# Optimization experiments

Hardware: AMD Instinct MI355X
Metric: run time of the kernel (lower is better)

## Reference

```python
import jax, jax.numpy as jnp
import numpy as np

B, L, N = 512, 512, 128


def setup_inputs() -> dict:
    key = jax.random.key(0)
    k1, k2, k3, k4 = jax.random.split(key, 4)
    emission = jax.random.normal(k1, (B, L, N), dtype=jnp.float32)
    target = jax.random.randint(k2, (B, L), 0, N, dtype=jnp.int32)
    mask = jnp.ones((B, L), dtype=jnp.float32)
    # params: uniform(-0.1, 0.1) as in reset_parameters
    start_trans = jax.random.uniform(k3, (N,), minval=-0.1, maxval=0.1, dtype=jnp.float32)
    trans = jax.random.uniform(k4, (N, N), minval=-0.1, maxval=0.1, dtype=jnp.float32)
    return {"emission": emission, "target": target, "mask": mask,
            "start_trans": start_trans, "trans": trans}


def _normalizer(emission, mask, start_trans, trans):
    # scores: [B, N]
    scores0 = start_trans + emission[:, 0]
    em_t = jnp.swapaxes(emission, 0, 1)[1:]          # [L-1, B, N]
    m_t = jnp.swapaxes(mask, 0, 1)[1:, :, None]      # [L-1, B, 1]

    def step(scores, xs):
        em_i, m_i = xs
        nxt = jax.nn.logsumexp(scores[:, :, None] + trans[None], axis=1) + em_i
        nxt = m_i * nxt + (1.0 - m_i) * scores
        return nxt, None

    final, _ = jax.lax.scan(step, scores0, (em_t, m_t))
    return jax.nn.logsumexp(final, axis=1)            # [B]


def _path_score(emission, target, mask, start_trans, trans):
    # mask*next + (1-mask)*scores == scores + mask*increment -> fully vectorizable
    b = jnp.arange(emission.shape[0])
    t0 = target[:, 0]
    s0 = start_trans[t0] + emission[b, 0, t0]                         # [B]
    prev, cur = target[:, :-1], target[:, 1:]                         # [B, L-1]
    em_gather = jnp.take_along_axis(emission[:, 1:], cur[:, :, None], axis=2)[..., 0]
    inc = trans[prev, cur] + em_gather                                # [B, L-1]
    return s0 + jnp.sum(mask[:, 1:] * inc, axis=1)                    # [B]


def reference(emission, target, mask, start_trans, trans):
    path_scores = _path_score(emission, target, mask, start_trans, trans)
    normalizer = _normalizer(emission, mask, start_trans, trans)
    return jnp.mean(normalizer - path_scores)
```

## Files before the change

### kernel.cpp

```cpp
#include <hip/hip_runtime.h>

#define B_ 512
#define L_ 512
#define N_ 128
#define TM 256
#define C_BIAS 3.0f

typedef _Float16 h2_t __attribute__((ext_vector_type(2)));
typedef _Float16 h8_t __attribute__((ext_vector_type(8)));
typedef float    f4_t __attribute__((ext_vector_type(4)));

#define DPP_STEP_MAX(v, ctrl)                                                   \
    {                                                                           \
        int _t = __builtin_amdgcn_update_dpp(__float_as_int(v),                 \
                    __float_as_int(v), ctrl, 0xf, 0xf, false);                  \
        v = fmaxf(v, __int_as_float(_t));                                       \
    }
#define DPP_STEP_ADD(v, ctrl)                                                   \
    {                                                                           \
        int _t = __builtin_amdgcn_update_dpp(__float_as_int(v),                 \
                    __float_as_int(v), ctrl, 0xf, 0xf, false);                  \
        v = v + __int_as_float(_t);                                             \
    }

__device__ __forceinline__ float wave_max(float v) {
    DPP_STEP_MAX(v, 0xB1);
    DPP_STEP_MAX(v, 0x4E);
    DPP_STEP_MAX(v, 0x141);
    DPP_STEP_MAX(v, 0x140);
    DPP_STEP_MAX(v, 0x142);
    DPP_STEP_MAX(v, 0x143);
    return __int_as_float(__builtin_amdgcn_readlane(__float_as_int(v), 63));
}
__device__ __forceinline__ float wave_sum(float v) {
    DPP_STEP_ADD(v, 0xB1);
    DPP_STEP_ADD(v, 0x4E);
    DPP_STEP_ADD(v, 0x141);
    DPP_STEP_ADD(v, 0x140);
    DPP_STEP_ADD(v, 0x142);
    DPP_STEP_ADD(v, 0x143);
    return __int_as_float(__builtin_amdgcn_readlane(__float_as_int(v), 63));
}

__global__ __launch_bounds__(64) void norm_kernel(
    const float* __restrict__ em, const int* __restrict__ tg,
    const float* __restrict__ mask, const float* __restrict__ st,
    const float* __restrict__ trans,
    float* __restrict__ alpha, float* __restrict__ beta,
    float* __restrict__ pathf, float* __restrict__ pathb)
{
    __shared__ __align__(16) _Float16 Eh[128];
    __shared__ __align__(8)  float    Sl[128];
    __shared__ float Mlds[TM];

    const int l  = threadIdx.x;
    const int c  = l & 15;
    const int h  = l >> 4;
    const int b  = blockIdx.x >> 1;
    const int bw = blockIdx.x & 1;
    const size_t base = (size_t)b * L_ * N_;
    const int bL = b * L_;

    if (bw == 0) {
        float pacc = 0.f;
        for (int t = 1 + l; t < TM; t += 64) {
            int cur  = tg[bL + t];
            int prev = tg[bL + t - 1];
            pacc += mask[bL + t] * (trans[prev * N_ + cur] + em[base + (size_t)t * N_ + cur]);
        }
        pacc = wave_sum(pacc);
        if (l == 0) {
            int t0 = tg[bL];
            pathf[b] = pacc + st[t0] + em[base + t0];
        }

#pragma unroll
        for (int k = 0; k < 4; ++k) Mlds[l + 64 * k] = mask[bL + l + 64 * k];

        h8_t Bf[8][4];
#pragma unroll
        for (int jt = 0; jt < 8; ++jt)
#pragma unroll
            for (int ks = 0; ks < 4; ++ks) {
                h8_t f;
#pragma unroll
                for (int e = 0; e < 8; ++e)
                    f[e] = (_Float16)__expf(trans[(32 * ks + 8 * h + e) * N_ + 16 * jt + c]);
                Bf[jt][ks] = f;
            }

        float2 e0 = *(const float2*)(em + base + 2 * l);
        float2 s2 = *(const float2*)(st + 2 * l);
        float ns0 = s2.x + e0.x;
        float ns1 = s2.y + e0.y;
        float Mprev = wave_max(fmaxf(ns0, ns1));
        {
            h2_t eo;
            eo[0] = (_Float16)__expf(ns0 - Mprev - C_BIAS);
            eo[1] = (_Float16)__expf(ns1 - Mprev - C_BIAS);
            ((h2_t*)Eh)[l] = eo;
        }

        float2 pipe0 = *(const float2*)(em + base + (size_t)1 * N_ + 2 * l);
        float2 pipe1 = *(const float2*)(em + base + (size_t)2 * N_ + 2 * l);
        float2 pipe2 = *(const float2*)(em + base + (size_t)3 * N_ + 2 * l);
        float2 pipe3 = *(const float2*)(em + base + (size_t)4 * N_ + 2 * l);

        auto step = [&](int t, float2& slot) {
            float2 emv = slot;
            int tpf = t + 4; if (tpf > TM - 1) tpf = TM - 1;
            slot = *(const float2*)(em + base + (size_t)tpf * N_ + 2 * l);
            float mk = Mlds[t];

            float mx = wave_max(fmaxf(ns0, ns1));

            const _Float16* Eb = (const _Float16*)Eh;
            h8_t A0 = *(const h8_t*)(Eb + 8 * h);
            h8_t A1 = *(const h8_t*)(Eb + 32 + 8 * h);
            h8_t A2 = *(const h8_t*)(Eb + 64 + 8 * h);
            h8_t A3 = *(const h8_t*)(Eb + 96 + 8 * h);

            f4_t z = {0.f, 0.f, 0.f, 0.f};
            f4_t acc[8];
#pragma unroll
            for (int jt = 0; jt < 8; ++jt) {
                f4_t a = __builtin_amdgcn_mfma_f32_16x16x32_f16(A0, Bf[jt][0], z, 0, 0, 0);
                a = __builtin_amdgcn_mfma_f32_16x16x32_f16(A1, Bf[jt][1], a, 0, 0, 0);
                a = __builtin_amdgcn_mfma_f32_16x16x32_f16(A2, Bf[jt][2], a, 0, 0, 0);
                a = __builtin_amdgcn_mfma_f32_16x16x32_f16(A3, Bf[jt][3], a, 0, 0, 0);
                acc[jt] = a;
            }
            if (l < 16) {
#pragma unroll
                for (int jt = 0; jt < 8; ++jt) Sl[16 * jt + c] = acc[jt][0];
            }
            float2 sv = *(const float2*)(Sl + 2 * l);

            float badd = Mprev + C_BIAS;
            float nxt0 = __logf(sv.x) + badd + emv.x;
            float nxt1 = __logf(sv.y) + badd + emv.y;
            float im = 1.f - mk;
            ns0 = mk * nxt0 + im * ns0;
            ns1 = mk * nxt1 + im * ns1;

            Mprev = mx;
            h2_t eo;
            eo[0] = (_Float16)__expf(ns0 - mx - C_BIAS);
            eo[1] = (_Float16)__expf(ns1 - mx - C_BIAS);
            ((h2_t*)Eh)[l] = eo;
        };

        for (int tt = 1; tt + 3 < TM; tt += 4) {
            step(tt    , pipe0);
            step(tt + 1, pipe1);
            step(tt + 2, pipe2);
            step(tt + 3, pipe3);
        }
        step(TM - 3, pipe0);
        step(TM - 2, pipe1);
        step(TM - 1, pipe2);

        *(float2*)(alpha + b * N_ + 2 * l) = make_float2(ns0, ns1);
    } else {
        float pacc = 0.f;
        for (int t = TM + l; t < L_; t += 64) {
            int cur  = tg[bL + t];
            int prev = tg[bL + t - 1];
            pacc += mask[bL + t] * (trans[prev * N_ + cur] + em[base + (size_t)t * N_ + cur]);
        }
        pacc = wave_sum(pacc);
        if (l == 0) pathb[b] = pacc;

#pragma unroll
        for (int k = 0; k < 4; ++k) Mlds[l + 64 * k] = mask[bL + TM + l + 64 * k];

        h8_t Bf[8][4];
#pragma unroll
        for (int it = 0; it < 8; ++it)
#pragma unroll
            for (int ks = 0; ks < 4; ++ks) {
                const float* p = trans + (size_t)(16 * it + c) * N_ + 32 * ks + 8 * h;
                float4 q0 = *(const float4*)p;
                float4 q1 = *(const float4*)(p + 4);
                h8_t f;
                f[0] = (_Float16)__expf(q0.x); f[1] = (_Float16)__expf(q0.y);
                f[2] = (_Float16)__expf(q0.z); f[3] = (_Float16)__expf(q0.w);
                f[4] = (_Float16)__expf(q1.x); f[5] = (_Float16)__expf(q1.y);
                f[6] = (_Float16)__expf(q1.z); f[7] = (_Float16)__expf(q1.w);
                Bf[it][ks] = f;
            }

        float2 e0 = *(const float2*)(em + base + (size_t)(L_ - 1) * N_ + 2 * l);
        float b0 = 0.f, b1 = 0.f;
        float v0 = e0.x, v1 = e0.y;
        float Mprev = wave_max(fmaxf(v0, v1));
        {
            h2_t eo;
            eo[0] = (_Float16)__expf(v0 - Mprev - C_BIAS);
            eo[1] = (_Float16)__expf(v1 - Mprev - C_BIAS);
            ((h2_t*)Eh)[l] = eo;
        }

        float2 pipe0 = *(const float2*)(em + base + (size_t)510 * N_ + 2 * l);
        float2 pipe1 = *(const float2*)(em + base + (size_t)509 * N_ + 2 * l);
        float2 pipe2 = *(const float2*)(em + base + (size_t)508 * N_ + 2 * l);
        float2 pipe3 = *(const float2*)(em + base + (size_t)507 * N_ + 2 * l);

        auto step = [&](int t, float2& slot) {
            float2 emt = slot;
            int tpf = t - 4; if (tpf < TM - 1) tpf = TM - 1;
            slot = *(const float2*)(em + base + (size_t)tpf * N_ + 2 * l);
            float mk = Mlds[t + 1 - TM];

            float mx = wave_max(fmaxf(v0, v1));

            const _Float16* Fb = (const _Float16*)Eh;
            h8_t A0 = *(const h8_t*)(Fb + 8 * h);
            h8_t A1 = *(const h8_t*)(Fb + 32 + 8 * h);
            h8_t A2 = *(const h8_t*)(Fb + 64 + 8 * h);
            h8_t A3 = *(const h8_t*)(Fb + 96 + 8 * h);

            f4_t z = {0.f, 0.f, 0.f, 0.f};
            f4_t acc[8];
#pragma unroll
            for (int it = 0; it < 8; ++it) {
                f4_t a = __builtin_amdgcn_mfma_f32_16x16x32_f16(A0, Bf[it][0], z, 0, 0, 0);
                a = __builtin_amdgcn_mfma_f32_16x16x32_f16(A1, Bf[it][1], a, 0, 0, 0);
                a = __builtin_amdgcn_mfma_f32_16x16x32_f16(A2, Bf[it][2], a, 0, 0, 0);
                a = __builtin_amdgcn_mfma_f32_16x16x32_f16(A3, Bf[it][3], a, 0, 0, 0);
                acc[it] = a;
            }
            if (l < 16) {
#pragma unroll
                for (int it = 0; it < 8; ++it) Sl[16 * it + c] = acc[it][0];
            }
            float2 sv = *(const float2*)(Sl + 2 * l);

            float badd = Mprev + C_BIAS;
            float upd0 = __logf(sv.x) + badd;
            float upd1 = __logf(sv.y) + badd;
            float im = 1.f - mk;
            b0 = mk * upd0 + im * b0;
            b1 = mk * upd1 + im * b1;

            v0 = b0 + emt.x;
            v1 = b1 + emt.y;
            Mprev = mx;
            h2_t eo;
            eo[0] = (_Float16)__expf(v0 - mx - C_BIAS);
            eo[1] = (_Float16)__expf(v1 - mx - C_BIAS);
            ((h2_t*)Eh)[l] = eo;
        };

        for (int tt = 510; tt >= 258; tt -= 4) {
            step(tt    , pipe0);
            step(tt - 1, pipe1);
            step(tt - 2, pipe2);
            step(tt - 3, pipe3);
        }

        *(float2*)(beta + b * N_ + 2 * l) = make_float2(b0, b1);
    }
}

__global__ __launch_bounds__(64) void zres_kernel(
    const float* __restrict__ alpha, const float* __restrict__ beta,
    const float* __restrict__ pathf, const float* __restrict__ pathb,
    float* __restrict__ zres)
{
    const int l = threadIdx.x;
    const int b = blockIdx.x;
    float2 av = *(const float2*)(alpha + b * N_ + 2 * l);
    float2 bv = *(const float2*)(beta  + b * N_ + 2 * l);
    float v0 = av.x + bv.x;
    float v1 = av.y + bv.y;
    float m = wave_max(fmaxf(v0, v1));
    float s = wave_sum(__expf(v0 - m) + __expf(v1 - m));
    if (l == 0) zres[b] = m + __logf(s) - pathf[b] - pathb[b];
}

__global__ __launch_bounds__(64) void mean_kernel(
    const float* __restrict__ zres, float* __restrict__ out)
{
    const int l = threadIdx.x;
    const float4* z4 = (const float4*)zres;
    float4 a = z4[2 * l];
    float4 c = z4[2 * l + 1];
    float acc = ((a.x + a.y) + (a.z + a.w)) + ((c.x + c.y) + (c.z + c.w));
    acc = wave_sum(acc);
    if (l == 0) out[0] = acc * (1.0f / (float)B_);
}

extern "C" void kernel_launch(void* const* d_in, const int* in_sizes, int n_in,
                              void* d_out, int out_size, void* d_ws, size_t ws_size,
                              hipStream_t stream) {
    const float* emission    = (const float*)d_in[0];
    const int*   target      = (const int*)  d_in[1];
    const float* mask        = (const float*)d_in[2];
    const float* start_trans = (const float*)d_in[3];
    const float* trans       = (const float*)d_in[4];
    float* out = (float*)d_out;

    float* ws_f  = (float*)d_ws;
    float* alpha = ws_f;
    float* beta  = ws_f + B_ * N_;
    float* pathf = ws_f + 2 * B_ * N_;
    float* pathb = ws_f + 2 * B_ * N_ + B_;
    float* zres  = ws_f + 2 * B_ * N_ + 2 * B_;

    norm_kernel<<<2 * B_, 64, 0, stream>>>(emission, target, mask, start_trans,
                                           trans, alpha, beta, pathf, pathb);
    zres_kernel<<<B_, 64, 0, stream>>>(alpha, beta, pathf, pathb, zres);
    mean_kernel<<<1, 64, 0, stream>>>(zres, out);
}
```

Before: 302.7 us.

## Remap state ownership to MFMA output layout, drop LDS round-trip for scores

Each lane now owns the two states (32*h+c and +16) that match the MFMA accumulator layout, so results are taken straight from the accumulator registers with selects. This removes the per-step LDS scatter of accumulator results and the gather that read them back, which sat on the serial recurrence path. Emission loads become scalar loads with a strided pattern instead of float2, and launch bounds add a min-blocks hint. In exchange, Eh writes become two half-word stores per lane.

New measurement: 307.7 us. About the same (+1.7%).

```diff
diff --git a/kernel.cpp b/kernel.cpp
--- a/kernel.cpp
+++ b/kernel.cpp
@@ -42,7 +42,13 @@
     return __int_as_float(__builtin_amdgcn_readlane(__float_as_int(v), 63));
 }
 
-__global__ __launch_bounds__(64) void norm_kernel(
+#define CHAIN4(qv, BT)                                                          \
+    f4_t qv = __builtin_amdgcn_mfma_f32_16x16x32_f16(A0, BT[0], z, 0, 0, 0);    \
+    qv = __builtin_amdgcn_mfma_f32_16x16x32_f16(A1, BT[1], qv, 0, 0, 0);        \
+    qv = __builtin_amdgcn_mfma_f32_16x16x32_f16(A2, BT[2], qv, 0, 0, 0);        \
+    qv = __builtin_amdgcn_mfma_f32_16x16x32_f16(A3, BT[3], qv, 0, 0, 0);
+
+__global__ __launch_bounds__(64, 1) void norm_kernel(
     const float* __restrict__ em, const int* __restrict__ tg,
     const float* __restrict__ mask, const float* __restrict__ st,
     const float* __restrict__ trans,
@@ -50,12 +56,15 @@
     float* __restrict__ pathf, float* __restrict__ pathb)
 {
     __shared__ __align__(16) _Float16 Eh[128];
-    __shared__ __align__(8)  float    Sl[128];
     __shared__ float Mlds[TM];
 
     const int l  = threadIdx.x;
     const int c  = l & 15;
     const int h  = l >> 4;
+    const int s0 = 32 * h + c;
+    const int s1 = s0 + 16;
+    const bool hb0 = (h & 1) != 0;
+    const bool hb1 = (h & 2) != 0;
     const int b  = blockIdx.x >> 1;
     const int bw = blockIdx.x & 1;
     const size_t base = (size_t)b * L_ * N_;
@@ -89,27 +98,22 @@
                 Bf[jt][ks] = f;
             }
 
-        float2 e0 = *(const float2*)(em + base + 2 * l);
-        float2 s2 = *(const float2*)(st + 2 * l);
-        float ns0 = s2.x + e0.x;
-        float ns1 = s2.y + e0.y;
+        float ns0 = st[s0] + em[base + s0];
+        float ns1 = st[s1] + em[base + s1];
         float Mprev = wave_max(fmaxf(ns0, ns1));
-        {
-            h2_t eo;
-            eo[0] = (_Float16)__expf(ns0 - Mprev - C_BIAS);
-            eo[1] = (_Float16)__expf(ns1 - Mprev - C_BIAS);
-            ((h2_t*)Eh)[l] = eo;
-        }
-
-        float2 pipe0 = *(const float2*)(em + base + (size_t)1 * N_ + 2 * l);
-        float2 pipe1 = *(const float2*)(em + base + (size_t)2 * N_ + 2 * l);
-        float2 pipe2 = *(const float2*)(em + base + (size_t)3 * N_ + 2 * l);
-        float2 pipe3 = *(const float2*)(em + base + (size_t)4 * N_ + 2 * l);
-
-        auto step = [&](int t, float2& slot) {
-            float2 emv = slot;
+        Eh[s0] = (_Float16)__expf(ns0 - Mprev - C_BIAS);
+        Eh[s1] = (_Float16)__expf(ns1 - Mprev - C_BIAS);
+
+        float pa0 = em[base + (size_t)1 * N_ + s0], pb0 = em[base + (size_t)1 * N_ + s1];
+        float pa1 = em[base + (size_t)2 * N_ + s0], pb1 = em[base + (size_t)2 * N_ + s1];
+        float pa2 = em[base + (size_t)3 * N_ + s0], pb2 = em[base + (size_t)3 * N_ + s1];
+        float pa3 = em[base + (size_t)4 * N_ + s0], pb3 = em[base + (size_t)4 * N_ + s1];
+
+        auto step = [&](int t, float& sa, float& sb) {
+            float emv0 = sa, emv1 = sb;
             int tpf = t + 4; if (tpf > TM - 1) tpf = TM - 1;
-            slot = *(const float2*)(em + base + (size_t)tpf * N_ + 2 * l);
+            sa = em[base + (size_t)tpf * N_ + s0];
+            sb = em[base + (size_t)tpf * N_ + s1];
             float mk = Mlds[t];
 
             float mx = wave_max(fmaxf(ns0, ns1));
@@ -121,46 +125,36 @@
             h8_t A3 = *(const h8_t*)(Eb + 96 + 8 * h);
 
             f4_t z = {0.f, 0.f, 0.f, 0.f};
-            f4_t acc[8];
-#pragma unroll
-            for (int jt = 0; jt < 8; ++jt) {
-                f4_t a = __builtin_amdgcn_mfma_f32_16x16x32_f16(A0, Bf[jt][0], z, 0, 0, 0);
-                a = __builtin_amdgcn_mfma_f32_16x16x32_f16(A1, Bf[jt][1], a, 0, 0, 0);
-                a = __builtin_amdgcn_mfma_f32_16x16x32_f16(A2, Bf[jt][2], a, 0, 0, 0);
-                a = __builtin_amdgcn_mfma_f32_16x16x32_f16(A3, Bf[jt][3], a, 0, 0, 0);
-                acc[jt] = a;
-            }
-            if (l < 16) {
-#pragma unroll
-                for (int jt = 0; jt < 8; ++jt) Sl[16 * jt + c] = acc[jt][0];
-            }
-            float2 sv = *(const float2*)(Sl + 2 * l);
+            CHAIN4(q0, Bf[0]) CHAIN4(q1, Bf[1]) CHAIN4(q2, Bf[2]) CHAIN4(q3, Bf[3])
+            CHAIN4(q4, Bf[4]) CHAIN4(q5, Bf[5]) CHAIN4(q6, Bf[6]) CHAIN4(q7, Bf[7])
+
+            float sv0 = hb1 ? (hb0 ? q6[0] : q4[0]) : (hb0 ? q2[0] : q0[0]);
+            float sv1 = hb1 ? (hb0 ? q7[0] : q5[0]) : (hb0 ? q3[0] : q1[0]);
 
             float badd = Mprev + C_BIAS;
-            float nxt0 = __logf(sv.x) + badd + emv.x;
-            float nxt1 = __logf(sv.y) + badd + emv.y;
+            float nxt0 = __logf(sv0) + badd + emv0;
+            float nxt1 = __logf(sv1) + badd + emv1;
             float im = 1.f - mk;
             ns0 = mk * nxt0 + im * ns0;
             ns1 = mk * nxt1 + im * ns1;
 
             Mprev = mx;
-            h2_t eo;
-            eo[0] = (_Float16)__expf(ns0 - mx - C_BIAS);
-            eo[1] = (_Float16)__expf(ns1 - mx - C_BIAS);
-            ((h2_t*)Eh)[l] = eo;
+            Eh[s0] = (_Float16)__expf(ns0 - mx - C_BIAS);
+            Eh[s1] = (_Float16)__expf(ns1 - mx - C_BIAS);
         };
 
         for (int tt = 1; tt + 3 < TM; tt += 4) {
-            step(tt    , pipe0);
-            step(tt + 1, pipe1);
-            step(tt + 2, pipe2);
-            step(tt + 3, pipe3);
-        }
-        step(TM - 3, pipe0);
-        step(TM - 2, pipe1);
-        step(TM - 1, pipe2);
-
-        *(float2*)(alpha + b * N_ + 2 * l) = make_float2(ns0, ns1);
+            step(tt    , pa0, pb0);
+            step(tt + 1, pa1, pb1);
+            step(tt + 2, pa2, pb2);
+            step(tt + 3, pa3, pb3);
+        }
+        step(TM - 3, pa0, pb0);
+        step(TM - 2, pa1, pb1);
+        step(TM - 1, pa2, pb2);
+
+        alpha[b * N_ + s0] = ns0;
+        alpha[b * N_ + s1] = ns1;
     } else {
         float pacc = 0.f;
         for (int t = TM + l; t < L_; t += 64) {
@@ -190,26 +184,23 @@
                 Bf[it][ks] = f;
             }
 
-        float2 e0 = *(const float2*)(em + base + (size_t)(L_ - 1) * N_ + 2 * l);
         float b0 = 0.f, b1 = 0.f;
-        float v0 = e0.x, v1 = e0.y;
+        float v0 = em[base + (size_t)(L_ - 1) * N_ + s0];
+        float v1 = em[base + (size_t)(L_ - 1) * N_ + s1];
         float Mprev = wave_max(fmaxf(v0, v1));
-        {
-            h2_t eo;
-            eo[0] = (_Float16)__expf(v0 - Mprev - C_BIAS);
-            eo[1] = (_Float16)__expf(v1 - Mprev - C_BIAS);
-            ((h2_t*)Eh)[l] = eo;
-        }
-
-        float2 pipe0 = *(const float2*)(em + base + (size_t)510 * N_ + 2 * l);
-        float2 pipe1 = *(const float2*)(em + base + (size_t)509 * N_ + 2 * l);
-        float2 pipe2 = *(const float2*)(em + base + (size_t)508 * N_ + 2 * l);
-        float2 pipe3 = *(const float2*)(em + base + (size_t)507 * N_ + 2 * l);
-
-        auto step = [&](int t, float2& slot) {
-            float2 emt = slot;
+        Eh[s0] = (_Float16)__expf(v0 - Mprev - C_BIAS);
+        Eh[s1] = (_Float16)__expf(v1 - Mprev - C_BIAS);
+
+        float pa0 = em[base + (size_t)510 * N_ + s0], pb0 = em[base + (size_t)510 * N_ + s1];
+        float pa1 = em[base + (size_t)509 * N_ + s0], pb1 = em[base + (size_t)509 * N_ + s1];
+        float pa2 = em[base + (size_t)508 * N_ + s0], pb2 = em[base + (size_t)508 * N_ + s1];
+        float pa3 = em[base + (size_t)507 * N_ + s0], pb3 = em[base + (size_t)507 * N_ + s1];
+
+        auto step = [&](int t, float& sa, float& sb) {
+            float emt0 = sa, emt1 = sb;
             int tpf = t - 4; if (tpf < TM - 1) tpf = TM - 1;
-            slot = *(const float2*)(em + base + (size_t)tpf * N_ + 2 * l);
+            sa = em[base + (size_t)tpf * N_ + s0];
+            sb = em[base + (size_t)tpf * N_ + s1];
             float mk = Mlds[t + 1 - TM];
 
             float mx = wave_max(fmaxf(v0, v1));
@@ -221,45 +212,35 @@
             h8_t A3 = *(const h8_t*)(Fb + 96 + 8 * h);
 
             f4_t z = {0.f, 0.f, 0.f, 0.f};
-            f4_t acc[8];
-#pragma unroll
-            for (int it = 0; it < 8; ++it) {
-                f4_t a = __builtin_amdgcn_mfma_f32_16x16x32_f16(A0, Bf[it][0], z, 0, 0, 0);
-                a = __builtin_amdgcn_mfma_f32_16x16x32_f16(A1, Bf[it][1], a, 0, 0, 0);
-                a = __builtin_amdgcn_mfma_f32_16x16x32_f16(A2, Bf[it][2], a, 0, 0, 0);
-                a = __builtin_amdgcn_mfma_f32_16x16x32_f16(A3, Bf[it][3], a, 0, 0, 0);
-                acc[it] = a;
-            }
-            if (l < 16) {
-#pragma unroll
-                for (int it = 0; it < 8; ++it) Sl[16 * it + c] = acc[it][0];
-            }
-            float2 sv = *(const float2*)(Sl + 2 * l);
+            CHAIN4(q0, Bf[0]) CHAIN4(q1, Bf[1]) CHAIN4(q2, Bf[2]) CHAIN4(q3, Bf[3])
+            CHAIN4(q4, Bf[4]) CHAIN4(q5, Bf[5]) CHAIN4(q6, Bf[6]) CHAIN4(q7, Bf[7])
+
+            float sv0 = hb1 ? (hb0 ? q6[0] : q4[0]) : (hb0 ? q2[0] : q0[0]);
+            float sv1 = hb1 ? (hb0 ? q7[0] : q5[0]) : (hb0 ? q3[0] : q1[0]);
 
             float badd = Mprev + C_BIAS;
-            float upd0 = __logf(sv.x) + badd;
-            float upd1 = __logf(sv.y) + badd;
+            float upd0 = __logf(sv0) + badd;
+            float upd1 = __logf(sv1) + badd;
             float im = 1.f - mk;
             b0 = mk * upd0 + im * b0;
             b1 = mk * upd1 + im * b1;
 
-            v0 = b0 + emt.x;
-            v1 = b1 + emt.y;
+            v0 = b0 + emt0;
+            v1 = b1 + emt1;
             Mprev = mx;
-            h2_t eo;
-            eo[0] = (_Float16)__expf(v0 - mx - C_BIAS);
-            eo[1] = (_Float16)__expf(v1 - mx - C_BIAS);
-            ((h2_t*)Eh)[l] = eo;
+            Eh[s0] = (_Float16)__expf(v0 - mx - C_BIAS);
+            Eh[s1] = (_Float16)__expf(v1 - mx - C_BIAS);
         };
 
         for (int tt = 510; tt >= 258; tt -= 4) {
-            step(tt    , pipe0);
-            step(tt - 1, pipe1);
-            step(tt - 2, pipe2);
-            step(tt - 3, pipe3);
-        }
-
-        *(float2*)(beta + b * N_ + 2 * l) = make_float2(b0, b1);
+            step(tt    , pa0, pb0);
+            step(tt - 1, pa1, pb1);
+            step(tt - 2, pa2, pb2);
+            step(tt - 3, pa3, pb3);
+        }
+
+        beta[b * N_ + s0] = b0;
+        beta[b * N_ + s1] = b1;
     }
 }
 
```
